# Optimization experiments

Hardware: AMD Instinct MI355X
Metric: run time of the kernel (lower is better)

Reference implementation:

```python
import jax, jax.numpy as jnp
import numpy as np

NEG_SLOPE = 0.2  # PyG GATConv default leaky_relu slope
N_NODES, N_EDGES, F_IN, HID = 25000, 200000, 64, 128


def gat_layer(x, src, dst, W, a_src, a_dst, b, heads, ch):
    """PyG-style GATConv (concat=True, eval mode). x:[N,Fin] -> [N,heads*ch]."""
    N = x.shape[0]
    h = (x @ W).reshape(N, heads, ch)                      # [N,H,C]
    al_s = jnp.sum(h * a_src, axis=-1)                     # [N,H]
    al_d = jnp.sum(h * a_dst, axis=-1)                     # [N,H]
    e = jax.nn.leaky_relu(al_s[src] + al_d[dst], NEG_SLOPE)  # [E,H]
    # segment softmax over incoming edges of each dst node (stable)
    e = e - jax.ops.segment_max(e, dst, num_segments=N)[dst]
    ex = jnp.exp(e)
    alpha = ex / jax.ops.segment_sum(ex, dst, num_segments=N)[dst]  # [E,H]
    out = jax.ops.segment_sum(h[src] * alpha[:, :, None], dst, num_segments=N)  # [N,H,C]
    return out.reshape(N, heads * ch) + b


def setup_inputs() -> dict:
    key = jax.random.key(0)
    ks = jax.random.split(key, 24)
    def g(k, shape, fan_in):
        return jax.random.normal(k, shape, dtype=jnp.float32) / np.sqrt(fan_in)
    inp = {
        "x": jax.random.normal(ks[0], (N_NODES, F_IN), dtype=jnp.float32),
        "edge_index": jax.random.randint(ks[1], (2, N_EDGES), 0, N_NODES, dtype=jnp.int64) if jax.config.jax_enable_x64 else jax.random.randint(ks[1], (2, N_EDGES), 0, N_NODES).astype(jnp.int32),
        "liquor_idx": jax.random.randint(ks[2], (4096,), 0, N_NODES),
        "ingredient_idx": jax.random.randint(ks[3], (4096,), 0, N_NODES),
        "W1": g(ks[4], (F_IN, 8 * HID), F_IN), "a_s1": g(ks[5], (8, HID), HID), "a_d1": g(ks[6], (8, HID), HID), "b1": jnp.zeros((8 * HID,), jnp.float32),
        "W2": g(ks[7], (8 * HID, 8 * HID), 8 * HID), "a_s2": g(ks[8], (8, HID), HID), "a_d2": g(ks[9], (8, HID), HID), "b2": jnp.zeros((8 * HID,), jnp.float32),
        "W3": g(ks[10], (8 * HID, HID), 8 * HID), "a_s3": g(ks[11], (1, HID), HID), "a_d3": g(ks[12], (1, HID), HID), "b3": jnp.zeros((HID,), jnp.float32),
        # MLP scorer: 256 -> 128 -> 64 -> 1
        "mw1": g(ks[13], (2 * HID, HID), 2 * HID), "mb1": jnp.zeros((HID,), jnp.float32),
        "mw2": g(ks[14], (HID, HID // 2), HID), "mb2": jnp.zeros((HID // 2,), jnp.float32),
        "mw3": g(ks[15], (HID // 2, 1), HID // 2), "mb3": jnp.zeros((1,), jnp.float32),
    }
    return inp


def reference(x, edge_index, liquor_idx, ingredient_idx,
              W1, a_s1, a_d1, b1, W2, a_s2, a_d2, b2, W3, a_s3, a_d3, b3,
              mw1, mb1, mw2, mb2, mw3, mb3):
    N = x.shape[0]
    loops = jnp.arange(N, dtype=edge_index.dtype)  # GATConv adds self-loops
    src = jnp.concatenate([edge_index[0], loops])
    dst = jnp.concatenate([edge_index[1], loops])
    h = jax.nn.relu(gat_layer(x, src, dst, W1, a_s1, a_d1, b1, 8, HID))
    h = jax.nn.relu(gat_layer(h, src, dst, W2, a_s2, a_d2, b2, 8, HID))
    h = gat_layer(h, src, dst, W3, a_s3, a_d3, b3, 1, HID)
    pair = jnp.concatenate([h[liquor_idx], h[ingredient_idx]], axis=-1)  # [B,256]
    z = jax.nn.relu(pair @ mw1 + mb1)
    z = jax.nn.relu(z @ mw2 + mb2)
    z = z @ mw3 + mb3
    return jax.nn.sigmoid(z).squeeze(-1)
```

## Files before the change

kernel.cpp:

```cpp
#include <hip/hip_runtime.h>
#include <math.h>

#define NEG_SLOPE 0.2f

typedef short short8 __attribute__((ext_vector_type(8)));
typedef float f32x4 __attribute__((ext_vector_type(4)));

__device__ __forceinline__ float lrelu(float x){ return x > 0.f ? x : NEG_SLOPE * x; }

__device__ __forceinline__ unsigned short f2bf(float f){
  union { float f; unsigned u; } v; v.f = f;
  unsigned r = v.u + 0x7fff + ((v.u >> 16) & 1);
  return (unsigned short)(r >> 16);
}
__device__ __forceinline__ float bf2f(unsigned short u){
  union { unsigned u; float f; } v; v.u = ((unsigned)u) << 16; return v.f;
}

__device__ __forceinline__ void gld16(const unsigned short* g, unsigned short* l){
  __builtin_amdgcn_global_load_lds(
      (const __attribute__((address_space(1))) unsigned int*)g,
      (__attribute__((address_space(3))) unsigned int*)l, 16, 0, 0);
}

__global__ void k_count(const int* __restrict__ dst, int* __restrict__ cnt, int E){
  int e = blockIdx.x*blockDim.x + threadIdx.x;
  if (e < E) atomicAdd(&cnt[dst[e]], 1);
}

__global__ void k_blockscan(const int* __restrict__ cnt, int* __restrict__ row,
                            int* __restrict__ aux, int n){
  __shared__ int buf[256];
  int t = threadIdx.x;
  int base = blockIdx.x * 256;
  int v = (base + t < n) ? cnt[base + t] : 0;
  buf[t] = v;
  __syncthreads();
  #pragma unroll
  for (int off = 1; off < 256; off <<= 1){
    int u = (t >= off) ? buf[t - off] : 0;
    __syncthreads();
    buf[t] += u;
    __syncthreads();
  }
  if (base + t < n) row[base + t + 1] = buf[t];
  if (t == 255) aux[blockIdx.x] = buf[255];
  if (blockIdx.x == 0 && t == 0) row[0] = 0;
}

__global__ void k_addoff(const int* __restrict__ aux, int* __restrict__ row, int n){
  __shared__ int s_pre;
  int b = blockIdx.x, t = threadIdx.x;
  if (t == 0){
    int pre = 0;
    for (int i = 0; i < b; ++i) pre += aux[i];
    s_pre = pre;
  }
  __syncthreads();
  int i = b * 256 + t;
  if (i < n) row[i + 1] += s_pre;
}

__global__ void k_scatter(const int* __restrict__ src, const int* __restrict__ dst,
                          const int* __restrict__ row, int* __restrict__ cur,
                          int* __restrict__ csr, int E){
  int e = blockIdx.x*blockDim.x + threadIdx.x;
  if (e < E){
    int d = dst[e];
    int p = atomicAdd(&cur[d], 1);
    csr[row[d] + p] = src[e];
  }
}

__global__ void k_prep(const float* __restrict__ x, unsigned short* __restrict__ xb, int nx, int nxb,
                       const float* __restrict__ W1, unsigned short* __restrict__ Wt1,
                       const float* __restrict__ W2, unsigned short* __restrict__ Wt2,
                       const float* __restrict__ W3, unsigned short* __restrict__ Wt3){
  __shared__ float tile[32][33];
  int b = blockIdx.x, t = threadIdx.x;
  if (b < nxb){
    int i0 = b * 2048 + t * 8;
    if (i0 + 8 <= nx){
      float4 f0 = *reinterpret_cast<const float4*>(x + i0);
      float4 f1 = *reinterpret_cast<const float4*>(x + i0 + 4);
      short8 o;
      o[0]=f2bf(f0.x); o[1]=f2bf(f0.y); o[2]=f2bf(f0.z); o[3]=f2bf(f0.w);
      o[4]=f2bf(f1.x); o[5]=f2bf(f1.y); o[6]=f2bf(f1.z); o[7]=f2bf(f1.w);
      *reinterpret_cast<short8*>(xb + i0) = o;
    } else {
      for (int k = 0; k < 8 && i0 + k < nx; ++k) xb[i0 + k] = f2bf(x[i0 + k]);
    }
    return;
  }
  const float* W; unsigned short* Wt; int K, N, ti;
  if (b < nxb + 64)            { W = W1; Wt = Wt1; K = 64;   N = 1024; ti = b - nxb;
                                 int kb = (ti & 1) * 32, nb = (ti >> 1) * 32;
                                 int tx = t & 31, ty = t >> 5;
                                 #pragma unroll
                                 for (int i = ty; i < 32; i += 8) tile[i][tx] = W[(size_t)(kb+i)*N + nb+tx];
                                 __syncthreads();
                                 #pragma unroll
                                 for (int i = ty; i < 32; i += 8) Wt[(size_t)(nb+i)*K + kb+tx] = f2bf(tile[tx][i]);
                                 return; }
  if (b < nxb + 64 + 1024)     { W = W2; Wt = Wt2; K = 1024; N = 1024; ti = b - nxb - 64; }
  else                         { W = W3; Wt = Wt3; K = 1024; N = 128;  ti = b - nxb - 64 - 1024; }
  int kb = (ti & 31) * 32, nb = (ti >> 5) * 32;
  int tx = t & 31, ty = t >> 5;
  #pragma unroll
  for (int i = ty; i < 32; i += 8) tile[i][tx] = W[(size_t)(kb+i)*N + nb+tx];
  __syncthreads();
  #pragma unroll
  for (int i = ty; i < 32; i += 8) Wt[(size_t)(nb+i)*K + kb+tx] = f2bf(tile[tx][i]);
}

__global__ void k_fold(const float* __restrict__ W1, const float* __restrict__ a_s,
                       const float* __restrict__ a_d, float* __restrict__ ws){
  int k = blockIdx.x, t = threadIdx.x;
  int h = t >> 5, l = t & 31;
  float4 wv = *reinterpret_cast<const float4*>(&W1[(size_t)k * 1024 + h * 128 + l * 4]);
  float4 sv = *reinterpret_cast<const float4*>(&a_s[h * 128 + l * 4]);
  float4 dv = *reinterpret_cast<const float4*>(&a_d[h * 128 + l * 4]);
  float ps = wv.x*sv.x + wv.y*sv.y + wv.z*sv.z + wv.w*sv.w;
  float pd = wv.x*dv.x + wv.y*dv.y + wv.z*dv.z + wv.w*dv.w;
  #pragma unroll
  for (int off = 16; off >= 1; off >>= 1){
    ps += __shfl_xor(ps, off);
    pd += __shfl_xor(pd, off);
  }
  if (l == 0){ ws[k * 16 + h] = ps; ws[k * 16 + 8 + h] = pd; }
}

__global__ void k_logits1(const unsigned short* __restrict__ xb, const float* __restrict__ ws,
                          float* __restrict__ ALS, float* __restrict__ ALD, int N){
  __shared__ unsigned short lx[32 * 64];
  __shared__ float lw[64 * 16];
  int t = threadIdx.x;
  int n0 = blockIdx.x * 32;
  int r = t >> 3, c = (t & 7) * 8;
  if (n0 + r < N)
    *reinterpret_cast<short8*>(&lx[r * 64 + c]) =
      *reinterpret_cast<const short8*>(&xb[(size_t)(n0 + r) * 64 + c]);
  else {
    short8 z = {0,0,0,0,0,0,0,0};
    *reinterpret_cast<short8*>(&lx[r * 64 + c]) = z;
  }
  *reinterpret_cast<float4*>(&lw[t * 4]) = *reinterpret_cast<const float4*>(&ws[t * 4]);
  __syncthreads();
  int nl = t >> 3, h = t & 7;
  if (n0 + nl >= N) return;
  float s = 0.f, d = 0.f;
  #pragma unroll 8
  for (int k = 0; k < 64; ++k){
    float xv = bf2f(lx[nl * 64 + k]);
    s = fmaf(xv, lw[k * 16 + h], s);
    d = fmaf(xv, lw[k * 16 + 8 + h], d);
  }
  ALS[(size_t)(n0 + nl) * 8 + h] = s;
  ALD[(size_t)(n0 + nl) * 8 + h] = d;
}

__global__ void k_gat_x(const unsigned short* __restrict__ xb, const float* __restrict__ ALS,
                        const float* __restrict__ ALD, const int* __restrict__ row,
                        const int* __restrict__ csr, unsigned short* __restrict__ G, int N){
  int t = threadIdx.x;
  int n = blockIdx.x * 4 + (t >> 6);
  if (n >= N) return;
  int lane = t & 63;
  float ald[8], m[8], l[8], acc[8];
  float xv = bf2f(xb[(size_t)n * 64 + lane]);
  #pragma unroll
  for (int h = 0; h < 8; ++h){
    ald[h] = ALD[(size_t)n * 8 + h];
    m[h] = lrelu(ALS[(size_t)n * 8 + h] + ald[h]);
    l[h] = 1.f;
    acc[h] = xv;
  }
  int beg = row[n], end = row[n + 1];
  for (int j = beg; j < end; ++j){
    int s = csr[j];
    float xs = bf2f(xb[(size_t)s * 64 + lane]);
    #pragma unroll
    for (int h = 0; h < 8; ++h){
      float e = lrelu(ALS[(size_t)s * 8 + h] + ald[h]);
      float mn = fmaxf(m[h], e);
      float sc = __expf(m[h] - mn);
      float p  = __expf(e - mn);
      acc[h] = acc[h] * sc + p * xs;
      l[h]   = l[h] * sc + p;
      m[h]   = mn;
    }
  }
  #pragma unroll
  for (int h = 0; h < 8; ++h)
    G[(size_t)n * 512 + h * 64 + lane] = f2bf(acc[h] / l[h]);
}

__global__ __launch_bounds__(256) void k_gemm_g(
    const unsigned short* __restrict__ G,
    const unsigned short* __restrict__ Bt,
    const float* __restrict__ bias,
    unsigned short* __restrict__ C,
    int M){
  __shared__ unsigned short As[128 * 32];
  __shared__ unsigned short Bs[128 * 32];
  const int nwg = gridDim.x;
  int bid = blockIdx.x;
  int swz = ((nwg & 7) == 0) ? ((bid & 7) * (nwg >> 3) + (bid >> 3)) : bid;
  const int head = swz % 8, byi = swz / 8;
  const int bm = byi * 128, bn = head * 128;
  const int tid  = threadIdx.x;
  const int lane = tid & 63, wave = tid >> 6;
  const int wr = wave >> 1, wc = wave & 1;
  const int lr = lane & 15, lk = lane >> 4;
  const int srow = wave * 16 + (lane >> 2);
  const int skc  = (lane & 3) * 8;
  int ar0 = bm + srow;      if (ar0 >= M) ar0 = M - 1;
  int ar1 = bm + srow + 64; if (ar1 >= M) ar1 = M - 1;
  const unsigned short* ga0 = G + (size_t)ar0 * 512 + head * 64 + skc;
  const unsigned short* ga1 = G + (size_t)ar1 * 512 + head * 64 + skc;
  const unsigned short* gb0 = Bt + (size_t)(bn + srow) * 64 + skc;
  const unsigned short* gb1 = Bt + (size_t)(bn + srow + 64) * 64 + skc;
  f32x4 acc[4][4] = {};
  #pragma unroll
  for (int k0 = 0; k0 < 64; k0 += 32){
    gld16(ga0 + k0, &As[(size_t)wave * 512]);
    gld16(ga1 + k0, &As[(size_t)(wave + 4) * 512]);
    gld16(gb0 + k0, &Bs[(size_t)wave * 512]);
    gld16(gb1 + k0, &Bs[(size_t)(wave + 4) * 512]);
    __syncthreads();
    short8 af[4], bg[4];
    #pragma unroll
    for (int m = 0; m < 4; ++m)
      af[m] = *reinterpret_cast<const short8*>(&As[(wr * 64 + m * 16 + lr) * 32 + lk * 8]);
    #pragma unroll
    for (int n = 0; n < 4; ++n)
      bg[n] = *reinterpret_cast<const short8*>(&Bs[(wc * 64 + n * 16 + lr) * 32 + lk * 8]);
    #pragma unroll
    for (int m = 0; m < 4; ++m)
      #pragma unroll
      for (int n = 0; n < 4; ++n)
        acc[m][n] = __builtin_amdgcn_mfma_f32_16x16x32_bf16(af[m], bg[n], acc[m][n], 0, 0, 0);
    __syncthreads();
  }
  float bv[4];
  #pragma unroll
  for (int n = 0; n < 4; ++n) bv[n] = bias[bn + wc * 64 + n * 16 + lr];
  #pragma unroll
  for (int m = 0; m < 4; ++m){
    #pragma unroll
    for (int j = 0; j < 4; ++j){
      int rowi = bm + wr * 64 + m * 16 + lk * 4 + j;
      if (rowi < M){
        #pragma unroll
        for (int n = 0; n < 4; ++n)
          C[(size_t)rowi * 1024 + bn + wc * 64 + n * 16 + lr] = f2bf(fmaxf(acc[m][n][j] + bv[n], 0.f));
      }
    }
  }
}

template<int HEADS>
__global__ __launch_bounds__(256) void k_gemm_fused(
    const unsigned short* __restrict__ A,
    const unsigned short* __restrict__ Bt,
    unsigned short* __restrict__ C,
    const float* __restrict__ a_s, const float* __restrict__ a_d,
    float* __restrict__ ALS, float* __restrict__ ALD,
    int M, int N, int K, int gxc){
  __shared__ unsigned short SMEM[2 * 128 * 32];
  unsigned short* As = SMEM;
  unsigned short* Bs = SMEM + 128 * 32;
  const int nwg = gridDim.x;
  int bid = blockIdx.x;
  int swz = ((nwg & 7) == 0) ? ((bid & 7) * (nwg >> 3) + (bid >> 3)) : bid;
  const int bxi = swz % gxc, byi = swz / gxc;
  const int bm = byi * 128, bn = bxi * 128;
  const int head = bxi;
  const int tid  = threadIdx.x;
  const int lane = tid & 63, wave = tid >> 6;
  const int wr = wave >> 1, wc = wave & 1;
  const int lr = lane & 15, lk = lane >> 4;
  const int srow = wave * 16 + (lane >> 2);
  const int skc  = (lane & 3) * 8;
  int ar0 = bm + srow;      if (ar0 >= M) ar0 = M - 1;
  int ar1 = bm + srow + 64; if (ar1 >= M) ar1 = M - 1;
  const unsigned short* ga0 = A  + (size_t)ar0 * K + skc;
  const unsigned short* ga1 = A  + (size_t)ar1 * K + skc;
  const unsigned short* gb0 = Bt + (size_t)(bn + srow) * K + skc;
  const unsigned short* gb1 = Bt + (size_t)(bn + srow + 64) * K + skc;
  f32x4 acc[4][4] = {};
  for (int k0 = 0; k0 < K; k0 += 32){
    gld16(ga0 + k0, &As[(size_t)wave * 512]);
    gld16(ga1 + k0, &As[(size_t)(wave + 4) * 512]);
    gld16(gb0 + k0, &Bs[(size_t)wave * 512]);
    gld16(gb1 + k0, &Bs[(size_t)(wave + 4) * 512]);
    __syncthreads();
    short8 af[4], bg[4];
    #pragma unroll
    for (int m = 0; m < 4; ++m)
      af[m] = *reinterpret_cast<const short8*>(&As[(wr * 64 + m * 16 + lr) * 32 + lk * 8]);
    #pragma unroll
    for (int n = 0; n < 4; ++n)
      bg[n] = *reinterpret_cast<const short8*>(&Bs[(wc * 64 + n * 16 + lr) * 32 + lk * 8]);
    #pragma unroll
    for (int m = 0; m < 4; ++m)
      #pragma unroll
      for (int n = 0; n < 4; ++n)
        acc[m][n] = __builtin_amdgcn_mfma_f32_16x16x32_bf16(af[m], bg[n], acc[m][n], 0, 0, 0);
    __syncthreads();
  }
  #pragma unroll
  for (int m = 0; m < 4; ++m){
    #pragma unroll
    for (int j = 0; j < 4; ++j){
      int rowi = bm + wr * 64 + m * 16 + lk * 4 + j;
      if (rowi < M){
        #pragma unroll
        for (int n = 0; n < 4; ++n)
          C[(size_t)rowi * N + bn + wc * 64 + n * 16 + lr] = f2bf(acc[m][n][j]);
      }
    }
  }
  float as4[4], ad4[4];
  #pragma unroll
  for (int n = 0; n < 4; ++n){
    as4[n] = a_s[head * 128 + wc * 64 + n * 16 + lr];
    ad4[n] = a_d[head * 128 + wc * 64 + n * 16 + lr];
  }
  float* red = (float*)SMEM;
  #pragma unroll
  for (int m = 0; m < 4; ++m){
    #pragma unroll
    for (int j = 0; j < 4; ++j){
      float ps = 0.f;
      #pragma unroll
      for (int n = 0; n < 4; ++n) ps = fmaf(acc[m][n][j], as4[n], ps);
      red[(wr * 64 + m * 16 + lk * 4 + j) * 32 + wc * 16 + lr] = ps;
    }
  }
  __syncthreads();
  if (tid < 128){
    float s = 0.f;
    #pragma unroll
    for (int i = 0; i < 32; ++i) s += red[tid * 32 + ((i + tid) & 31)];
    int gr = bm + tid;
    if (gr < M) ALS[(size_t)gr * HEADS + head] = s;
  }
  __syncthreads();
  #pragma unroll
  for (int m = 0; m < 4; ++m){
    #pragma unroll
    for (int j = 0; j < 4; ++j){
      float pd = 0.f;
      #pragma unroll
      for (int n = 0; n < 4; ++n) pd = fmaf(acc[m][n][j], ad4[n], pd);
      red[(wr * 64 + m * 16 + lk * 4 + j) * 32 + wc * 16 + lr] = pd;
    }
  }
  __syncthreads();
  if (tid < 128){
    float s = 0.f;
    #pragma unroll
    for (int i = 0; i < 32; ++i) s += red[tid * 32 + ((i + tid) & 31)];
    int gr = bm + tid;
    if (gr < M) ALD[(size_t)gr * HEADS + head] = s;
  }
}

__global__ __launch_bounds__(512, 2) void k_gemm256(
    const unsigned short* __restrict__ A,
    const unsigned short* __restrict__ Bt,
    unsigned short* __restrict__ C,
    const float* __restrict__ a_s, const float* __restrict__ a_d,
    float* __restrict__ ALS, float* __restrict__ ALD,
    int M, int N, int K, int gxc){
  __shared__ unsigned short smem[2 * 24576];
  const int nwg = gridDim.x;
  int bid = blockIdx.x;
  int swz = ((nwg & 7) == 0) ? ((bid & 7) * (nwg >> 3) + (bid >> 3)) : bid;
  const int bxi = swz % gxc, byi = swz / gxc;
  const int bm = byi * 256, bn = bxi * 128, head = bxi;
  const int tid = threadIdx.x;
  const int lane = tid & 63, wave = tid >> 6;
  const int wr = wave >> 1, wc = wave & 1;
  const int lr = lane & 15, lk = lane >> 4;
  const int sr   = tid >> 3;
  const int scol = ((tid & 7) << 3) ^ ((sr & 7) << 3);
  size_t offA[4], offB[2];
  #pragma unroll
  for (int u = 0; u < 4; ++u){
    int r = bm + u * 64 + sr; if (r >= M) r = M - 1;
    offA[u] = (size_t)r * K + scol;
  }
  #pragma unroll
  for (int u = 0; u < 2; ++u)
    offB[u] = (size_t)(bn + u * 64 + sr) * K + scol;
  const int wdst = (tid >> 6) * 512;

  f32x4 acc[4][4] = {};
  short8 af[4][2], bg[4][2];
  const int NKT = K >> 6;
  const int rsw = (lr & 7) << 3;

  #pragma unroll
  for (int u = 0; u < 4; ++u) gld16(A + offA[u], &smem[u * 4096 + wdst]);
  #pragma unroll
  for (int u = 0; u < 2; ++u) gld16(Bt + offB[u], &smem[16384 + u * 4096 + wdst]);
  #pragma unroll
  for (int u = 0; u < 4; ++u) gld16(A + offA[u] + 64, &smem[24576 + u * 4096 + wdst]);
  asm volatile("s_waitcnt vmcnt(4)" ::: "memory");
  __builtin_amdgcn_s_barrier();

  for (int kt = 0; kt < NKT; ++kt){
    const int s = kt & 1;
    const unsigned short* sa = &smem[s * 24576];
    const unsigned short* sb = &smem[s * 24576 + 16384];
    #pragma unroll
    for (int m = 0; m < 4; ++m){
      int r = (wr * 64 + m * 16 + lr) * 64;
      af[m][0] = *reinterpret_cast<const short8*>(&sa[r + ((lk * 8) ^ rsw)]);
      af[m][1] = *reinterpret_cast<const short8*>(&sa[r + ((32 + lk * 8) ^ rsw)]);
    }
    #pragma unroll
    for (int n = 0; n < 2; ++n){
      int r = (wc * 64 + n * 16 + lr) * 64;
      bg[n][0] = *reinterpret_cast<const short8*>(&sb[r + ((lk * 8) ^ rsw)]);
      bg[n][1] = *reinterpret_cast<const short8*>(&sb[r + ((32 + lk * 8) ^ rsw)]);
    }
    if (kt + 1 < NKT){
      int so = (s ^ 1) * 24576 + 16384;
      gld16(Bt + offB[0] + (size_t)(kt + 1) * 64, &smem[so + wdst]);
      gld16(Bt + offB[1] + (size_t)(kt + 1) * 64, &smem[so + 4096 + wdst]);
    }
    __builtin_amdgcn_s_barrier();
    asm volatile("s_waitcnt lgkmcnt(0)" ::: "memory");
    __builtin_amdgcn_sched_barrier(0);
    __builtin_amdgcn_s_setprio(1);
    #pragma unroll
    for (int m = 0; m < 4; ++m)
      #pragma unroll
      for (int n = 0; n < 2; ++n){
        acc[m][n] = __builtin_amdgcn_mfma_f32_16x16x32_bf16(af[m][0], bg[n][0], acc[m][n], 0, 0, 0);
        acc[m][n] = __builtin_amdgcn_mfma_f32_16x16x32_bf16(af[m][1], bg[n][1], acc[m][n], 0, 0, 0);
      }
    __builtin_amdgcn_s_setprio(0);
    __builtin_amdgcn_s_barrier();
    #pragma unroll
    for (int n = 2; n < 4; ++n){
      int r = (wc * 64 + n * 16 + lr) * 64;
      bg[n][0] = *reinterpret_cast<const short8*>(&sb[r + ((lk * 8) ^ rsw)]);
      bg[n][1] = *reinterpret_cast<const short8*>(&sb[r + ((32 + lk * 8) ^ rsw)]);
    }
    if (kt + 2 < NKT){
      int so = s * 24576;
      #pragma unroll
      for (int u = 0; u < 4; ++u)
        gld16(A + offA[u] + (size_t)(kt + 2) * 64, &smem[so + u * 4096 + wdst]);
    }
    __builtin_amdgcn_s_barrier();
    asm volatile("s_waitcnt lgkmcnt(0)" ::: "memory");
    __builtin_amdgcn_sched_barrier(0);
    __builtin_amdgcn_s_setprio(1);
    #pragma unroll
    for (int m = 0; m < 4; ++m)
      #pragma unroll
      for (int n = 2; n < 4; ++n){
        acc[m][n] = __builtin_amdgcn_mfma_f32_16x16x32_bf16(af[m][0], bg[n][0], acc[m][n], 0, 0, 0);
        acc[m][n] = __builtin_amdgcn_mfma_f32_16x16x32_bf16(af[m][1], bg[n][1], acc[m][n], 0, 0, 0);
      }
    __builtin_amdgcn_s_setprio(0);
    asm volatile("s_waitcnt vmcnt(4)" ::: "memory");
    __builtin_amdgcn_s_barrier();
  }

  #pragma unroll
  for (int m = 0; m < 4; ++m)
    #pragma unroll
    for (int j = 0; j < 4; ++j){
      int row = bm + wr * 64 + m * 16 + lk * 4 + j;
      if (row < M){
        #pragma unroll
        for (int n = 0; n < 4; ++n)
          C[(size_t)row * N + bn + wc * 64 + n * 16 + lr] = f2bf(acc[m][n][j]);
      }
    }
  float as4[4], ad4[4];
  #pragma unroll
  for (int n = 0; n < 4; ++n){
    as4[n] = a_s[head * 128 + wc * 64 + n * 16 + lr];
    ad4[n] = a_d[head * 128 + wc * 64 + n * 16 + lr];
  }
  asm volatile("s_waitcnt vmcnt(0)" ::: "memory");
  __builtin_amdgcn_s_barrier();
  float2* red = (float2*)smem;
  #pragma unroll
  for (int m = 0; m < 4; ++m)
    #pragma unroll
    for (int j = 0; j < 4; ++j){
      float ps = 0.f, pd = 0.f;
      #pragma unroll
      for (int n = 0; n < 4; ++n){
        ps = fmaf(acc[m][n][j], as4[n], ps);
        pd = fmaf(acc[m][n][j], ad4[n], pd);
      }
      red[(wr * 64 + m * 16 + lk * 4 + j) * 32 + wc * 16 + lr] = make_float2(ps, pd);
    }
  __syncthreads();
  if (tid < 256){
    float ss = 0.f, sd = 0.f;
    #pragma unroll
    for (int i = 0; i < 32; ++i){
      float2 v = red[tid * 32 + ((i + tid) & 31)];
      ss += v.x; sd += v.y;
    }
    int gr = bm + tid;
    if (gr < M){
      ALS[(size_t)gr * 8 + head] = ss;
      ALD[(size_t)gr * 8 + head] = sd;
    }
  }
}

template<int HEADS, int VEC, int OUTBF>
__global__ void k_gat_bf(const unsigned short* __restrict__ hp, const float* __restrict__ al_s,
                         const float* __restrict__ al_d, const int* __restrict__ row,
                         const int* __restrict__ csr, const float* __restrict__ bias,
                         void* __restrict__ outv, int N, int do_relu){
  constexpr int TPH = 128 / VEC;
  int n = blockIdx.x;
  int t = threadIdx.x;
  int h = t / TPH;
  int c0 = (t % TPH) * VEC;
  float ald = al_d[(size_t)n * HEADS + h];
  float mA = lrelu(al_s[(size_t)n * HEADS + h] + ald);
  float lA = 1.f;
  float accA[VEC], accB[VEC];
  float mB = -1e30f, lB = 0.f;
  const unsigned short* hpn = hp + ((size_t)n * HEADS + h) * 128 + c0;
  if constexpr (VEC == 8){
    short8 hv8 = *reinterpret_cast<const short8*>(hpn);
    #pragma unroll
    for (int v = 0; v < 8; ++v){ accA[v] = bf2f((unsigned short)hv8[v]); accB[v] = 0.f; }
  } else {
    ushort2 hv2 = *reinterpret_cast<const ushort2*>(hpn);
    accA[0] = bf2f(hv2.x); accA[1] = bf2f(hv2.y);
    accB[0] = 0.f; accB[1] = 0.f;
  }
  int beg = row[n], end = row[n + 1];
  int j = beg;
  for (; j + 1 < end; j += 2){
    int s0 = csr[j], s1 = csr[j + 1];
    float e0 = lrelu(al_s[(size_t)s0 * HEADS + h] + ald);
    float e1 = lrelu(al_s[(size_t)s1 * HEADS + h] + ald);
    const unsigned short* p0 = hp + ((size_t)s0 * HEADS + h) * 128 + c0;
    const unsigned short* p1 = hp + ((size_t)s1 * HEADS + h) * 128 + c0;
    if constexpr (VEC == 8){
      short8 v0 = *reinterpret_cast<const short8*>(p0);
      short8 v1 = *reinterpret_cast<const short8*>(p1);
      float mn0 = fmaxf(mA, e0), mn1 = fmaxf(mB, e1);
      float sc0 = __expf(mA - mn0), sc1 = __expf(mB - mn1);
      float pw0 = __expf(e0 - mn0), pw1 = __expf(e1 - mn1);
      #pragma unroll
      for (int v = 0; v < 8; ++v){
        accA[v] = accA[v] * sc0 + pw0 * bf2f((unsigned short)v0[v]);
        accB[v] = accB[v] * sc1 + pw1 * bf2f((unsigned short)v1[v]);
      }
      lA = lA * sc0 + pw0; mA = mn0;
      lB = lB * sc1 + pw1; mB = mn1;
    } else {
      ushort2 v0 = *reinterpret_cast<const ushort2*>(p0);
      ushort2 v1 = *reinterpret_cast<const ushort2*>(p1);
      float mn0 = fmaxf(mA, e0), mn1 = fmaxf(mB, e1);
      float sc0 = __expf(mA - mn0), sc1 = __expf(mB - mn1);
      float pw0 = __expf(e0 - mn0), pw1 = __expf(e1 - mn1);
      accA[0] = accA[0] * sc0 + pw0 * bf2f(v0.x);
      accA[1] = accA[1] * sc0 + pw0 * bf2f(v0.y);
      accB[0] = accB[0] * sc1 + pw1 * bf2f(v1.x);
      accB[1] = accB[1] * sc1 + pw1 * bf2f(v1.y);
      lA = lA * sc0 + pw0; mA = mn0;
      lB = lB * sc1 + pw1; mB = mn1;
    }
  }
  if (j < end){
    int s0 = csr[j];
    float e0 = lrelu(al_s[(size_t)s0 * HEADS + h] + ald);
    const unsigned short* p0 = hp + ((size_t)s0 * HEADS + h) * 128 + c0;
    float mn0 = fmaxf(mA, e0);
    float sc0 = __expf(mA - mn0), pw0 = __expf(e0 - mn0);
    if constexpr (VEC == 8){
      short8 v0 = *reinterpret_cast<const short8*>(p0);
      #pragma unroll
      for (int v = 0; v < 8; ++v) accA[v] = accA[v] * sc0 + pw0 * bf2f((unsigned short)v0[v]);
    } else {
      ushort2 v0 = *reinterpret_cast<const ushort2*>(p0);
      accA[0] = accA[0] * sc0 + pw0 * bf2f(v0.x);
      accA[1] = accA[1] * sc0 + pw0 * bf2f(v0.y);
    }
    lA = lA * sc0 + pw0; mA = mn0;
  }
  float mn = fmaxf(mA, mB);
  float sA = __expf(mA - mn), sB = __expf(mB - mn);
  float l = lA * sA + lB * sB;
  float inv = 1.f / l;
  size_t ob = ((size_t)n * HEADS + h) * 128 + c0;
  #pragma unroll
  for (int v = 0; v < VEC; ++v){
    float o = (accA[v] * sA + accB[v] * sB) * inv + bias[h * 128 + c0 + v];
    if (do_relu) o = fmaxf(o, 0.f);
    if constexpr (OUTBF) ((unsigned short*)outv)[ob + v] = f2bf(o);
    else                 ((float*)outv)[ob + v] = o;
  }
}

__global__ void k_mlp(const float* __restrict__ h3, const int* __restrict__ liq,
                      const int* __restrict__ ing,
                      const float* __restrict__ mw1, const float* __restrict__ mb1,
                      const float* __restrict__ mw2, const float* __restrict__ mb2,
                      const float* __restrict__ mw3, const float* __restrict__ mb3,
                      float* __restrict__ out, int B){
  __shared__ float pairv[256];
  __shared__ float z1[128];
  __shared__ float z2[64];
  int r = blockIdx.x;
  int t = threadIdx.x;
  pairv[t]       = h3[(size_t)liq[r] * 128 + t];
  pairv[128 + t] = h3[(size_t)ing[r] * 128 + t];
  __syncthreads();
  float a1 = mb1[t];
  for (int k = 0; k < 256; ++k) a1 = fmaf(pairv[k], mw1[k * 128 + t], a1);
  z1[t] = fmaxf(a1, 0.f);
  __syncthreads();
  if (t < 64){
    float a2 = mb2[t];
    for (int k = 0; k < 128; ++k) a2 = fmaf(z1[k], mw2[k * 64 + t], a2);
    z2[t] = fmaxf(a2, 0.f);
  }
  __syncthreads();
  if (t < 64){
    float p = z2[t] * mw3[t];
    #pragma unroll
    for (int off = 32; off >= 1; off >>= 1) p += __shfl_xor(p, off);
    if (t == 0) out[r] = 1.f / (1.f + __expf(-(p + mb3[0])));
  }
}

extern "C" void kernel_launch(void* const* d_in, const int* in_sizes, int n_in,
                              void* d_out, int out_size, void* d_ws, size_t ws_size,
                              hipStream_t stream){
  const float* x   = (const float*)d_in[0];
  const int*   ei  = (const int*)  d_in[1];
  const int*   liq = (const int*)  d_in[2];
  const int*   ing = (const int*)  d_in[3];
  const float* W1  = (const float*)d_in[4];
  const float* as1 = (const float*)d_in[5];
  const float* ad1 = (const float*)d_in[6];
  const float* b1  = (const float*)d_in[7];
  const float* W2  = (const float*)d_in[8];
  const float* as2 = (const float*)d_in[9];
  const float* ad2 = (const float*)d_in[10];
  const float* b2  = (const float*)d_in[11];
  const float* W3  = (const float*)d_in[12];
  const float* as3 = (const float*)d_in[13];
  const float* ad3 = (const float*)d_in[14];
  const float* b3  = (const float*)d_in[15];
  const float* mw1 = (const float*)d_in[16];
  const float* mb1 = (const float*)d_in[17];
  const float* mw2 = (const float*)d_in[18];
  const float* mb2 = (const float*)d_in[19];
  const float* mw3 = (const float*)d_in[20];
  const float* mb3 = (const float*)d_in[21];
  float* out = (float*)d_out;

  const int N = in_sizes[0] / 64;
  const int E = in_sizes[1] / 2;
  const int B = in_sizes[2];
  const int* srcp = ei;
  const int* dstp = ei + E;

  char* w = (char*)d_ws;
  auto alloc = [&](size_t bytes) -> char* {
    char* p = w;
    w += (bytes + 255) & ~(size_t)255;
    return p;
  };
  unsigned short* P    = (unsigned short*)alloc((size_t)N * 1024 * 2);
  unsigned short* Hb   = (unsigned short*)alloc((size_t)N * 1024 * 2);
  float*          H3   = (float*)         alloc((size_t)N * 128 * 4);
  unsigned short* xb   = (unsigned short*)alloc((size_t)N * 64 * 2);
  unsigned short* Wt1  = (unsigned short*)alloc((size_t)1024 * 64 * 2);
  unsigned short* Wt2  = (unsigned short*)alloc((size_t)1024 * 1024 * 2);
  unsigned short* Wt3  = (unsigned short*)alloc((size_t)128 * 1024 * 2);
  float* ALS  = (float*)alloc((size_t)N * 8 * 4);
  float* ALD  = (float*)alloc((size_t)N * 8 * 4);
  float* ws1  = (float*)alloc((size_t)64 * 16 * 4);
  int*   row  = (int*)  alloc((size_t)(N + 1) * 4);
  int*   cntcur = (int*)alloc((size_t)2 * N * 4);
  int*   cnt  = cntcur;
  int*   cur  = cntcur + N;
  int*   aux  = (int*)  alloc((size_t)256 * 4);
  int*   csr  = (int*)  alloc((size_t)E * 4);
  unsigned short* G = P;
  (void)ws_size; (void)n_in; (void)out_size;

  int nx = N * 64;
  int nxb = (nx + 2047) / 2048;
  k_prep<<<nxb + 64 + 1024 + 128, 256, 0, stream>>>(x, xb, nx, nxb, W1, Wt1, W2, Wt2, W3, Wt3);
  k_fold<<<64, 256, 0, stream>>>(W1, as1, ad1, ws1);

  hipMemsetAsync(cntcur, 0, (size_t)2 * N * 4, stream);
  int eb = (E + 255) / 256;
  int nb = (N + 255) / 256;
  k_count<<<eb, 256, 0, stream>>>(dstp, cnt, E);
  k_blockscan<<<nb, 256, 0, stream>>>(cnt, row, aux, N);
  k_addoff<<<nb, 256, 0, stream>>>(aux, row, N);
  k_scatter<<<eb, 256, 0, stream>>>(srcp, dstp, row, cur, csr, E);

  const int mt  = (N + 127) / 128;
  const int mt2 = (N + 255) / 256;

  k_logits1<<<(N + 31) / 32, 256, 0, stream>>>(xb, ws1, ALS, ALD, N);
  k_gat_x<<<(N + 3) / 4, 256, 0, stream>>>(xb, ALS, ALD, row, csr, G, N);
  k_gemm_g<<<8 * mt, 256, 0, stream>>>(G, Wt1, b1, Hb, N);

  k_gemm256<<<8 * mt2, 512, 0, stream>>>(Hb, Wt2, P, as2, ad2, ALS, ALD, N, 1024, 1024, 8);
  k_gat_bf<8,8,1><<<N, 128, 0, stream>>>(P, ALS, ALD, row, csr, b2, Hb, N, 1);

  k_gemm_fused<1><<<1 * mt, 256, 0, stream>>>(Hb, Wt3, P, as3, ad3, ALS, ALD, N, 128, 1024, 1);
  k_gat_bf<1,2,0><<<N, 64, 0, stream>>>(P, ALS, ALD, row, csr, b3, H3, N, 0);

  k_mlp<<<B, 128, 0, stream>>>(H3, liq, ing, mw1, mb1, mw2, mb2, mw3, mb3, out, B);
}
```

Before: 353.7 us.

## Widen layer-2 GEMM tile to 256x256 and compute layer-3 aggregation only for queried nodes

The layer-2 GEMM now uses a 256x256 output tile with 8 waves arranged 2x4. Each block covers two heads and computes both heads' attention logits in two reduction passes. The K loop is unrolled by two with finer-grained interleaving of LDS reads, global-to-LDS loads and MFMA quads, aiming for more operand reuse per byte loaded. Separately, the final GAT aggregation runs only for the 2*B nodes indexed by liquor/ingredient, using a new online-softmax kernel, instead of for all N nodes. This cuts layer-3 aggregation work, at the cost of higher register pressure in the GEMM (32 accumulators) and an extra reduction pass in its epilogue.

```diff
diff --git a/kernel.cpp b/kernel.cpp
--- a/kernel.cpp
+++ b/kernel.cpp
@@ -22,6 +22,8 @@
       (const __attribute__((address_space(1))) unsigned int*)g,
       (__attribute__((address_space(3))) unsigned int*)l, 16, 0, 0);
 }
+
+#define MFMA_BF16 __builtin_amdgcn_mfma_f32_16x16x32_bf16
 
 __global__ void k_count(const int* __restrict__ dst, int* __restrict__ cnt, int E){
   int e = blockIdx.x*blockDim.x + threadIdx.x;
@@ -239,7 +241,7 @@
     for (int m = 0; m < 4; ++m)
       #pragma unroll
       for (int n = 0; n < 4; ++n)
-        acc[m][n] = __builtin_amdgcn_mfma_f32_16x16x32_bf16(af[m], bg[n], acc[m][n], 0, 0, 0);
+        acc[m][n] = MFMA_BF16(af[m], bg[n], acc[m][n], 0, 0, 0);
     __syncthreads();
   }
   float bv[4];
@@ -261,8 +263,7 @@
 
 template<int HEADS>
 __global__ __launch_bounds__(256) void k_gemm_fused(
-    const unsigned short* __restrict__ A,
-    const unsigned short* __restrict__ Bt,
+    const unsigned short* __restrict__ A, const unsigned short* __restrict__ Bt,
     unsigned short* __restrict__ C,
     const float* __restrict__ a_s, const float* __restrict__ a_d,
     float* __restrict__ ALS, float* __restrict__ ALD,
@@ -306,7 +307,7 @@
     for (int m = 0; m < 4; ++m)
       #pragma unroll
       for (int n = 0; n < 4; ++n)
-        acc[m][n] = __builtin_amdgcn_mfma_f32_16x16x32_bf16(af[m], bg[n], acc[m][n], 0, 0, 0);
+        acc[m][n] = MFMA_BF16(af[m], bg[n], acc[m][n], 0, 0, 0);
     __syncthreads();
   }
   #pragma unroll
@@ -367,158 +368,189 @@
   }
 }
 
-__global__ __launch_bounds__(512, 2) void k_gemm256(
+__global__ __launch_bounds__(512, 2) void k_gemm256p8(
     const unsigned short* __restrict__ A,
     const unsigned short* __restrict__ Bt,
     unsigned short* __restrict__ C,
     const float* __restrict__ a_s, const float* __restrict__ a_d,
     float* __restrict__ ALS, float* __restrict__ ALD,
     int M, int N, int K, int gxc){
-  __shared__ unsigned short smem[2 * 24576];
+  __shared__ unsigned short smem[2 * 32768];
   const int nwg = gridDim.x;
   int bid = blockIdx.x;
   int swz = ((nwg & 7) == 0) ? ((bid & 7) * (nwg >> 3) + (bid >> 3)) : bid;
   const int bxi = swz % gxc, byi = swz / gxc;
-  const int bm = byi * 256, bn = bxi * 128, head = bxi;
+  const int bm = byi * 256, bn = bxi * 256;
   const int tid = threadIdx.x;
   const int lane = tid & 63, wave = tid >> 6;
-  const int wr = wave >> 1, wc = wave & 1;
+  const int wr = wave >> 2, wc = wave & 3;
   const int lr = lane & 15, lk = lane >> 4;
-  const int sr   = tid >> 3;
+  const int sr = tid >> 3;
   const int scol = ((tid & 7) << 3) ^ ((sr & 7) << 3);
-  size_t offA[4], offB[2];
+  unsigned offA[4], offB[4];
   #pragma unroll
   for (int u = 0; u < 4; ++u){
     int r = bm + u * 64 + sr; if (r >= M) r = M - 1;
-    offA[u] = (size_t)r * K + scol;
-  }
-  #pragma unroll
-  for (int u = 0; u < 2; ++u)
-    offB[u] = (size_t)(bn + u * 64 + sr) * K + scol;
-  const int wdst = (tid >> 6) * 512;
-
-  f32x4 acc[4][4] = {};
-  short8 af[4][2], bg[4][2];
+    offA[u] = (unsigned)r * (unsigned)K + scol;
+    offB[u] = (unsigned)(bn + u * 64 + sr) * (unsigned)K + scol;
+  }
+  const int wdst = wave * 512;
   const int NKT = K >> 6;
-  const int rsw = (lr & 7) << 3;
-
-  #pragma unroll
-  for (int u = 0; u < 4; ++u) gld16(A + offA[u], &smem[u * 4096 + wdst]);
-  #pragma unroll
-  for (int u = 0; u < 2; ++u) gld16(Bt + offB[u], &smem[16384 + u * 4096 + wdst]);
-  #pragma unroll
-  for (int u = 0; u < 4; ++u) gld16(A + offA[u] + 64, &smem[24576 + u * 4096 + wdst]);
+  const int NIT = NKT >> 1;
+
+  #define STA(T,u) gld16(A  + (size_t)offA[u] + (size_t)(T)*64, &smem[((T)&1)*32768 + (u)*4096 + wdst])
+  #define STB(T,u) gld16(Bt + (size_t)offB[u] + (size_t)(T)*64, &smem[((T)&1)*32768 + 16384 + (u)*4096 + wdst])
+
+  #pragma unroll
+  for (int u = 0; u < 4; ++u) STA(0, u);
+  #pragma unroll
+  for (int u = 0; u < 4; ++u) STB(0, u);
+  #pragma unroll
+  for (int u = 0; u < 4; ++u) STA(1, u);
   asm volatile("s_waitcnt vmcnt(4)" ::: "memory");
   __builtin_amdgcn_s_barrier();
 
-  for (int kt = 0; kt < NKT; ++kt){
-    const int s = kt & 1;
-    const unsigned short* sa = &smem[s * 24576];
-    const unsigned short* sb = &smem[s * 24576 + 16384];
-    #pragma unroll
-    for (int m = 0; m < 4; ++m){
-      int r = (wr * 64 + m * 16 + lr) * 64;
-      af[m][0] = *reinterpret_cast<const short8*>(&sa[r + ((lk * 8) ^ rsw)]);
-      af[m][1] = *reinterpret_cast<const short8*>(&sa[r + ((32 + lk * 8) ^ rsw)]);
-    }
-    #pragma unroll
-    for (int n = 0; n < 2; ++n){
-      int r = (wc * 64 + n * 16 + lr) * 64;
-      bg[n][0] = *reinterpret_cast<const short8*>(&sb[r + ((lk * 8) ^ rsw)]);
-      bg[n][1] = *reinterpret_cast<const short8*>(&sb[r + ((32 + lk * 8) ^ rsw)]);
-    }
-    if (kt + 1 < NKT){
-      int so = (s ^ 1) * 24576 + 16384;
-      gld16(Bt + offB[0] + (size_t)(kt + 1) * 64, &smem[so + wdst]);
-      gld16(Bt + offB[1] + (size_t)(kt + 1) * 64, &smem[so + 4096 + wdst]);
-    }
+  f32x4 acc[8][4] = {};
+  short8 af[4][2], bg[4][2];
+
+  #define RD_A(moff) \
+    _Pragma("unroll") \
+    for (int m = 0; m < 4; ++m){ \
+      int row = wr * 128 + (m + (moff)) * 16 + lr; \
+      int rb = row * 64, sw = (row & 7) << 3; \
+      af[m][0] = *reinterpret_cast<const short8*>(&sa[rb + ((lk * 8) ^ sw)]); \
+      af[m][1] = *reinterpret_cast<const short8*>(&sa[rb + ((32 + lk * 8) ^ sw)]); \
+    }
+  #define RD_B(n0_, n1_) \
+    _Pragma("unroll") \
+    for (int n = (n0_); n < (n1_); ++n){ \
+      int row = wc * 64 + n * 16 + lr; \
+      int rb = row * 64, sw = (row & 7) << 3; \
+      bg[n][0] = *reinterpret_cast<const short8*>(&sb[rb + ((lk * 8) ^ sw)]); \
+      bg[n][1] = *reinterpret_cast<const short8*>(&sb[rb + ((32 + lk * 8) ^ sw)]); \
+    }
+  #define SYNC_MFMA_BEG \
+    __builtin_amdgcn_s_barrier(); \
+    asm volatile("s_waitcnt lgkmcnt(0)" ::: "memory"); \
+    __builtin_amdgcn_sched_barrier(0); \
+    __builtin_amdgcn_s_setprio(1);
+  #define QUAD(mb, nb) \
+    _Pragma("unroll") \
+    for (int m = 0; m < 4; ++m) \
+      _Pragma("unroll") \
+      for (int n = 0; n < 2; ++n){ \
+        acc[(mb)+m][(nb)+n] = MFMA_BF16(af[m][0], bg[(nb)+n][0], acc[(mb)+m][(nb)+n], 0, 0, 0); \
+        acc[(mb)+m][(nb)+n] = MFMA_BF16(af[m][1], bg[(nb)+n][1], acc[(mb)+m][(nb)+n], 0, 0, 0); \
+      }
+  #define SYNC_MFMA_END \
+    __builtin_amdgcn_s_setprio(0); \
     __builtin_amdgcn_s_barrier();
-    asm volatile("s_waitcnt lgkmcnt(0)" ::: "memory");
-    __builtin_amdgcn_sched_barrier(0);
-    __builtin_amdgcn_s_setprio(1);
-    #pragma unroll
-    for (int m = 0; m < 4; ++m)
-      #pragma unroll
-      for (int n = 0; n < 2; ++n){
-        acc[m][n] = __builtin_amdgcn_mfma_f32_16x16x32_bf16(af[m][0], bg[n][0], acc[m][n], 0, 0, 0);
-        acc[m][n] = __builtin_amdgcn_mfma_f32_16x16x32_bf16(af[m][1], bg[n][1], acc[m][n], 0, 0, 0);
-      }
-    __builtin_amdgcn_s_setprio(0);
-    __builtin_amdgcn_s_barrier();
-    #pragma unroll
-    for (int n = 2; n < 4; ++n){
-      int r = (wc * 64 + n * 16 + lr) * 64;
-      bg[n][0] = *reinterpret_cast<const short8*>(&sb[r + ((lk * 8) ^ rsw)]);
-      bg[n][1] = *reinterpret_cast<const short8*>(&sb[r + ((32 + lk * 8) ^ rsw)]);
-    }
-    if (kt + 2 < NKT){
-      int so = s * 24576;
-      #pragma unroll
-      for (int u = 0; u < 4; ++u)
-        gld16(A + offA[u] + (size_t)(kt + 2) * 64, &smem[so + u * 4096 + wdst]);
-    }
-    __builtin_amdgcn_s_barrier();
-    asm volatile("s_waitcnt lgkmcnt(0)" ::: "memory");
-    __builtin_amdgcn_sched_barrier(0);
-    __builtin_amdgcn_s_setprio(1);
-    #pragma unroll
-    for (int m = 0; m < 4; ++m)
-      #pragma unroll
-      for (int n = 2; n < 4; ++n){
-        acc[m][n] = __builtin_amdgcn_mfma_f32_16x16x32_bf16(af[m][0], bg[n][0], acc[m][n], 0, 0, 0);
-        acc[m][n] = __builtin_amdgcn_mfma_f32_16x16x32_bf16(af[m][1], bg[n][1], acc[m][n], 0, 0, 0);
-      }
-    __builtin_amdgcn_s_setprio(0);
-    asm volatile("s_waitcnt vmcnt(4)" ::: "memory");
-    __builtin_amdgcn_s_barrier();
-  }
-
-  #pragma unroll
-  for (int m = 0; m < 4; ++m)
+
+  for (int it = 0; it < NIT; ++it){
+    const int T = it << 1;
+    {
+      const unsigned short* sa = &smem[(T & 1) * 32768];
+      const unsigned short* sb = sa + 16384;
+      RD_A(0); RD_B(0, 2);
+      STB(T + 1, 0); STB(T + 1, 1);
+      SYNC_MFMA_BEG; QUAD(0, 0); SYNC_MFMA_END;
+      RD_B(2, 4);
+      STB(T + 1, 2); STB(T + 1, 3);
+      SYNC_MFMA_BEG; QUAD(0, 2); SYNC_MFMA_END;
+      RD_A(4);
+      if (T + 2 < NKT){ STA(T + 2, 0); STA(T + 2, 2); }
+      SYNC_MFMA_BEG; QUAD(4, 0); SYNC_MFMA_END;
+      if (T + 2 < NKT){ STA(T + 2, 1); STA(T + 2, 3); }
+      __builtin_amdgcn_s_barrier();
+      __builtin_amdgcn_s_setprio(1);
+      QUAD(4, 2);
+      __builtin_amdgcn_s_setprio(0);
+      asm volatile("s_waitcnt vmcnt(4)" ::: "memory");
+      __builtin_amdgcn_s_barrier();
+    }
+    {
+      const unsigned short* sa = &smem[((T + 1) & 1) * 32768];
+      const unsigned short* sb = sa + 16384;
+      RD_A(0); RD_B(0, 2);
+      if (T + 2 < NKT){ STB(T + 2, 0); STB(T + 2, 1); }
+      SYNC_MFMA_BEG; QUAD(0, 0); SYNC_MFMA_END;
+      RD_B(2, 4);
+      if (T + 2 < NKT){ STB(T + 2, 2); STB(T + 2, 3); }
+      SYNC_MFMA_BEG; QUAD(0, 2); SYNC_MFMA_END;
+      RD_A(4);
+      if (T + 3 < NKT){ STA(T + 3, 0); STA(T + 3, 2); }
+      SYNC_MFMA_BEG; QUAD(4, 0); SYNC_MFMA_END;
+      if (T + 3 < NKT){ STA(T + 3, 1); STA(T + 3, 3); }
+      __builtin_amdgcn_s_barrier();
+      __builtin_amdgcn_s_setprio(1);
+      QUAD(4, 2);
+      __builtin_amdgcn_s_setprio(0);
+      asm volatile("s_waitcnt vmcnt(4)" ::: "memory");
+      __builtin_amdgcn_s_barrier();
+    }
+  }
+
+  #pragma unroll
+  for (int m = 0; m < 8; ++m){
     #pragma unroll
     for (int j = 0; j < 4; ++j){
-      int row = bm + wr * 64 + m * 16 + lk * 4 + j;
+      int row = bm + wr * 128 + m * 16 + lk * 4 + j;
       if (row < M){
         #pragma unroll
         for (int n = 0; n < 4; ++n)
           C[(size_t)row * N + bn + wc * 64 + n * 16 + lr] = f2bf(acc[m][n][j]);
       }
     }
+  }
+  const int hloc = wc >> 1;
   float as4[4], ad4[4];
   #pragma unroll
   for (int n = 0; n < 4; ++n){
-    as4[n] = a_s[head * 128 + wc * 64 + n * 16 + lr];
-    ad4[n] = a_d[head * 128 + wc * 64 + n * 16 + lr];
-  }
-  asm volatile("s_waitcnt vmcnt(0)" ::: "memory");
-  __builtin_amdgcn_s_barrier();
+    as4[n] = a_s[(bxi * 2 + hloc) * 128 + (wc & 1) * 64 + n * 16 + lr];
+    ad4[n] = a_d[(bxi * 2 + hloc) * 128 + (wc & 1) * 64 + n * 16 + lr];
+  }
   float2* red = (float2*)smem;
-  #pragma unroll
-  for (int m = 0; m < 4; ++m)
-    #pragma unroll
-    for (int j = 0; j < 4; ++j){
-      float ps = 0.f, pd = 0.f;
+  __syncthreads();
+  #pragma unroll
+  for (int hh = 0; hh < 2; ++hh){
+    if (hloc == hh){
       #pragma unroll
-      for (int n = 0; n < 4; ++n){
-        ps = fmaf(acc[m][n][j], as4[n], ps);
-        pd = fmaf(acc[m][n][j], ad4[n], pd);
+      for (int m = 0; m < 8; ++m){
+        #pragma unroll
+        for (int j = 0; j < 4; ++j){
+          float ps = 0.f, pd = 0.f;
+          #pragma unroll
+          for (int n = 0; n < 4; ++n){
+            ps = fmaf(acc[m][n][j], as4[n], ps);
+            pd = fmaf(acc[m][n][j], ad4[n], pd);
+          }
+          red[(wr * 128 + m * 16 + lk * 4 + j) * 32 + (wc & 1) * 16 + lr] = make_float2(ps, pd);
+        }
       }
-      red[(wr * 64 + m * 16 + lk * 4 + j) * 32 + wc * 16 + lr] = make_float2(ps, pd);
-    }
-  __syncthreads();
-  if (tid < 256){
-    float ss = 0.f, sd = 0.f;
-    #pragma unroll
-    for (int i = 0; i < 32; ++i){
-      float2 v = red[tid * 32 + ((i + tid) & 31)];
-      ss += v.x; sd += v.y;
-    }
-    int gr = bm + tid;
-    if (gr < M){
-      ALS[(size_t)gr * 8 + head] = ss;
-      ALD[(size_t)gr * 8 + head] = sd;
-    }
-  }
+    }
+    __syncthreads();
+    if (tid < 256){
+      float ss = 0.f, sd = 0.f;
+      #pragma unroll
+      for (int i = 0; i < 32; ++i){
+        float2 v = red[tid * 32 + ((i + tid) & 31)];
+        ss += v.x; sd += v.y;
+      }
+      int gr = bm + tid;
+      if (gr < M){
+        ALS[(size_t)gr * 8 + bxi * 2 + hh] = ss;
+        ALD[(size_t)gr * 8 + bxi * 2 + hh] = sd;
+      }
+    }
+    __syncthreads();
+  }
+  #undef STA
+  #undef STB
+  #undef RD_A
+  #undef RD_B
+  #undef SYNC_MFMA_BEG
+  #undef QUAD
+  #undef SYNC_MFMA_END
 }
 
 template<int HEADS, int VEC, int OUTBF>
@@ -612,8 +644,38 @@
   }
 }
 
-__global__ void k_mlp(const float* __restrict__ h3, const int* __restrict__ liq,
-                      const int* __restrict__ ing,
+__global__ void k_gat3(const unsigned short* __restrict__ hp, const float* __restrict__ al_s,
+                       const float* __restrict__ al_d, const int* __restrict__ row,
+                       const int* __restrict__ csr, const float* __restrict__ bias,
+                       const int* __restrict__ liq, const int* __restrict__ ing,
+                       float* __restrict__ out, int NB){
+  int b = blockIdx.x;
+  int n = (b < NB) ? liq[b] : ing[b - NB];
+  int t = threadIdx.x;
+  int c0 = t * 2;
+  float ald = al_d[n];
+  float m = lrelu(al_s[n] + ald);
+  float l = 1.f;
+  ushort2 hv2 = *reinterpret_cast<const ushort2*>(hp + (size_t)n * 128 + c0);
+  float a0 = bf2f(hv2.x), a1 = bf2f(hv2.y);
+  int beg = row[n], end = row[n + 1];
+  for (int j = beg; j < end; ++j){
+    int s = csr[j];
+    float e = lrelu(al_s[s] + ald);
+    float mn = fmaxf(m, e);
+    float sc = __expf(m - mn), p = __expf(e - mn);
+    ushort2 v = *reinterpret_cast<const ushort2*>(hp + (size_t)s * 128 + c0);
+    a0 = a0 * sc + p * bf2f(v.x);
+    a1 = a1 * sc + p * bf2f(v.y);
+    l = l * sc + p;
+    m = mn;
+  }
+  float inv = 1.f / l;
+  out[(size_t)b * 128 + c0]     = a0 * inv + bias[c0];
+  out[(size_t)b * 128 + c0 + 1] = a1 * inv + bias[c0 + 1];
+}
+
+__global__ void k_mlp(const float* __restrict__ h3,
                       const float* __restrict__ mw1, const float* __restrict__ mb1,
                       const float* __restrict__ mw2, const float* __restrict__ mb2,
                       const float* __restrict__ mw3, const float* __restrict__ mb3,
@@ -623,8 +685,8 @@
   __shared__ float z2[64];
   int r = blockIdx.x;
   int t = threadIdx.x;
-  pairv[t]       = h3[(size_t)liq[r] * 128 + t];
-  pairv[128 + t] = h3[(size_t)ing[r] * 128 + t];
+  pairv[t]       = h3[(size_t)r * 128 + t];
+  pairv[128 + t] = h3[(size_t)(B + r) * 128 + t];
   __syncthreads();
   float a1 = mb1[t];
   for (int k = 0; k < 256; ++k) a1 = fmaf(pairv[k], mw1[k * 128 + t], a1);
@@ -685,7 +747,7 @@
   };
   unsigned short* P    = (unsigned short*)alloc((size_t)N * 1024 * 2);
   unsigned short* Hb   = (unsigned short*)alloc((size_t)N * 1024 * 2);
-  float*          H3   = (float*)         alloc((size_t)N * 128 * 4);
+  float*          H3   = (float*)         alloc((size_t)2 * B * 128 * 4);
   unsigned short* xb   = (unsigned short*)alloc((size_t)N * 64 * 2);
   unsigned short* Wt1  = (unsigned short*)alloc((size_t)1024 * 64 * 2);
   unsigned short* Wt2  = (unsigned short*)alloc((size_t)1024 * 1024 * 2);
@@ -722,11 +784,11 @@
   k_gat_x<<<(N + 3) / 4, 256, 0, stream>>>(xb, ALS, ALD, row, csr, G, N);
   k_gemm_g<<<8 * mt, 256, 0, stream>>>(G, Wt1, b1, Hb, N);
 
-  k_gemm256<<<8 * mt2, 512, 0, stream>>>(Hb, Wt2, P, as2, ad2, ALS, ALD, N, 1024, 1024, 8);
+  k_gemm256p8<<<4 * mt2, 512, 0, stream>>>(Hb, Wt2, P, as2, ad2, ALS, ALD, N, 1024, 1024, 4);
   k_gat_bf<8,8,1><<<N, 128, 0, stream>>>(P, ALS, ALD, row, csr, b2, Hb, N, 1);
 
   k_gemm_fused<1><<<1 * mt, 256, 0, stream>>>(Hb, Wt3, P, as3, ad3, ALS, ALD, N, 128, 1024, 1);
-  k_gat_bf<1,2,0><<<N, 64, 0, stream>>>(P, ALS, ALD, row, csr, b3, H3, N, 0);
-
-  k_mlp<<<B, 128, 0, stream>>>(H3, liq, ing, mw1, mb1, mw2, mb2, mw3, mb3, out, B);
-}
+  k_gat3<<<2 * B, 64, 0, stream>>>(P, ALS, ALD, row, csr, b3, liq, ing, H3, B);
+
+  k_mlp<<<B, 128, 0, stream>>>(H3, mw1, mb1, mw2, mb2, mw3, mb3, out, B);
+}
```

After: 333.2 us. 1.06x faster.
